# Performance work log

Measured on AMD Instinct MI355X. Metric: run time of the kernel, lower is better.

Reference implementation:

```python
import jax, jax.numpy as jnp
import numpy as np

D_MODEL = 1024
NUM_HEADS = 16
D_K = D_MODEL // NUM_HEADS
B, S = 2, 2048


def setup_inputs() -> dict:
    key = jax.random.key(0)
    ks = jax.random.split(key, 12)
    s = 1.0 / np.sqrt(D_MODEL)
    return {
        "query": jax.random.normal(ks[0], (B, S, D_MODEL), jnp.float32),
        "key": jax.random.normal(ks[1], (B, S, D_MODEL), jnp.float32),
        "value": jax.random.normal(ks[2], (B, S, D_MODEL), jnp.float32),
        "mask": jnp.ones((B, S), jnp.int32),
        "Wq": jax.random.uniform(ks[3], (D_MODEL, D_MODEL), jnp.float32, -s, s),
        "bq": jax.random.uniform(ks[4], (D_MODEL,), jnp.float32, -s, s),
        "Wk": jax.random.uniform(ks[5], (D_MODEL, D_MODEL), jnp.float32, -s, s),
        "bk": jax.random.uniform(ks[6], (D_MODEL,), jnp.float32, -s, s),
        "Wv": jax.random.uniform(ks[7], (D_MODEL, D_MODEL), jnp.float32, -s, s),
        "bv": jax.random.uniform(ks[8], (D_MODEL,), jnp.float32, -s, s),
        "Wo": jax.random.uniform(ks[9], (D_MODEL, D_MODEL), jnp.float32, -s, s),
        "bo": jax.random.uniform(ks[10], (D_MODEL,), jnp.float32, -s, s),
    }


def reference(query, key, value, mask, Wq, bq, Wk, bk, Wv, bv, Wo, bo):
    b, s, _ = query.shape
    scale = jnp.sqrt(jnp.asarray(D_K, jnp.float32)).astype(query.dtype)
    # QKV projections: x @ W.T + b (torch nn.Linear convention)
    Q = (query @ Wq.T + bq).reshape(b, s, NUM_HEADS, D_K).transpose(0, 2, 1, 3)
    K = (key @ Wk.T + bk).reshape(b, -1, NUM_HEADS, D_K).transpose(0, 2, 1, 3)
    V = (value @ Wv.T + bv).reshape(b, -1, NUM_HEADS, D_K).transpose(0, 2, 1, 3)
    # scores in fp32, then cast back to input dtype (matches source)
    scores = jnp.einsum('bhqd,bhkd->bhqk', Q.astype(jnp.float32), K.astype(jnp.float32)) / scale
    scores = scores.astype(Q.dtype)
    # 2D mask [B,S] -> [B,1,1,S], broadcast over heads/queries
    fill = jnp.finfo(scores.dtype).min
    scores = jnp.where(mask[:, None, None, :] == 0, fill, scores)
    attn = jax.nn.softmax(scores, axis=-1)  # dropout p=0 -> identity
    context = jnp.einsum('bhqk,bhkd->bhqd', attn, V)
    context = context.transpose(0, 2, 1, 3).reshape(b, s, D_MODEL)
    return context @ Wo.T + bo
```

## Files before the change

kernel.cpp:

```cpp
#include <hip/hip_runtime.h>


typedef __bf16 bf16_8 __attribute__((ext_vector_type(8)));
typedef float  f32x4  __attribute__((ext_vector_type(4)));
typedef float  f32x16 __attribute__((ext_vector_type(16)));
typedef unsigned int u32x4 __attribute__((ext_vector_type(4)));

#define MFMA16(a, b, c) __builtin_amdgcn_mfma_f32_16x16x32_bf16((a), (b), (c), 0, 0, 0)
#define MFMA32(a, b, c) __builtin_amdgcn_mfma_f32_32x32x16_bf16((a), (b), (c), 0, 0, 0)

__device__ __forceinline__ void async_ld16(const void* g, void* l) {
  __builtin_amdgcn_global_load_lds(
      (__attribute__((address_space(1))) void*)g,
      (__attribute__((address_space(3))) void*)l, 16, 0, 0);
}

__device__ __forceinline__ void gemm_core_128(
    const __bf16* __restrict__ A, const __bf16* __restrict__ BT, int K,
    int tm, int tn, __bf16* At, __bf16* Bt, f32x4 acc[4][4]) {
  const int tid  = threadIdx.x;
  const int lane = tid & 63;
  const int w    = tid >> 6;
  const int quad = lane >> 4;
  const int c16  = lane & 15;
  const int wm = w >> 1, wn = w & 1;

  const int ch0  = w * 2;
  const int row0 = ch0 * 16 + (lane >> 2);
  const int col0 = (lane & 3) * 8;
  const __bf16* Ag = A  + (size_t)(tm + row0) * K + col0;
  const __bf16* Bg = BT + (size_t)(tn + row0) * K + col0;
  __bf16* Al = At + ch0 * 512;
  __bf16* Bl = Bt + ch0 * 512;
  const size_t rowK16 = (size_t)16 * K;

  for (int kt = 0; kt < K; kt += 32) {
    async_ld16(Ag + kt,          Al);
    async_ld16(Ag + rowK16 + kt, Al + 512);
    async_ld16(Bg + kt,          Bl);
    async_ld16(Bg + rowK16 + kt, Bl + 512);
    __syncthreads();

    bf16_8 af[4], bfr[4];
#pragma unroll
    for (int mi = 0; mi < 4; ++mi)
      af[mi] = *(const bf16_8*)(At + (wm * 64 + mi * 16 + c16) * 32 + quad * 8);
#pragma unroll
    for (int ni = 0; ni < 4; ++ni)
      bfr[ni] = *(const bf16_8*)(Bt + (wn * 64 + ni * 16 + c16) * 32 + quad * 8);
#pragma unroll
    for (int mi = 0; mi < 4; ++mi)
#pragma unroll
      for (int ni = 0; ni < 4; ++ni)
        acc[mi][ni] = MFMA16(af[mi], bfr[ni], acc[mi][ni]);
    __syncthreads();
  }
}

__global__ __launch_bounds__(256)
void qkv_fused(const __bf16* __restrict__ xq, const __bf16* __restrict__ xk,
               const __bf16* __restrict__ xv,
               const __bf16* __restrict__ wq, const __bf16* __restrict__ wk,
               const __bf16* __restrict__ wv,
               const float* __restrict__ bq, const float* __restrict__ bk,
               const float* __restrict__ bv,
               __bf16* __restrict__ Qo, __bf16* __restrict__ Ko,
               __bf16* __restrict__ Vo) {
  __shared__ __bf16 At[128 * 32];
  __shared__ __bf16 Bt[128 * 32];
  const int z  = blockIdx.z;
  const int bx = blockIdx.x;
  const __bf16 *A, *BT;
  const float* bias;
  int tm, tn;
  if (z == 2) {
    A = wv; BT = xv; bias = bv;
    tm = (bx >> 5) * 128; tn = (bx & 31) * 128;
  } else if (z == 1) {
    A = xk; BT = wk; bias = bk;
    tm = (bx >> 3) * 128; tn = (bx & 7) * 128;
  } else {
    A = xq; BT = wq; bias = bq;
    tm = (bx >> 3) * 128; tn = (bx & 7) * 128;
  }

  f32x4 acc[4][4];
  const f32x4 zero4 = {0.f, 0.f, 0.f, 0.f};
#pragma unroll
  for (int i = 0; i < 4; ++i)
#pragma unroll
    for (int j = 0; j < 4; ++j) acc[i][j] = zero4;

  gemm_core_128(A, BT, 1024, tm, tn, At, Bt, acc);

  const int lane = threadIdx.x & 63;
  const int w    = threadIdx.x >> 6;
  const int quad = lane >> 4, c16 = lane & 15;
  const int wm = w >> 1, wn = w & 1;

  if (z == 2) {
#pragma unroll
    for (int mi = 0; mi < 4; ++mi) {
#pragma unroll
      for (int ni = 0; ni < 4; ++ni) {
        const int n  = tn + wn * 64 + ni * 16 + c16;
        const int bb = n >> 11, s = n & 2047;
#pragma unroll
        for (int r = 0; r < 4; ++r) {
          const int m  = tm + wm * 64 + mi * 16 + quad * 4 + r;
          const int hh = m >> 6, d = m & 63;
          Vo[(((size_t)(bb * 16 + hh) * 64 + d) << 11) + s] =
              (__bf16)(acc[mi][ni][r] + bias[m]);
        }
      }
    }
  } else {
    __bf16* Out = (z == 1) ? Ko : Qo;
    const float scale = (z == 0) ? 0.125f : 1.0f;
#pragma unroll
    for (int mi = 0; mi < 4; ++mi) {
#pragma unroll
      for (int ni = 0; ni < 4; ++ni) {
        const int n  = tn + wn * 64 + ni * 16 + c16;
        const int hh = n >> 6, d = n & 63;
        const float bn = bias[n];
#pragma unroll
        for (int r = 0; r < 4; ++r) {
          const int m  = tm + wm * 64 + mi * 16 + quad * 4 + r;
          const int bb = m >> 11, s = m & 2047;
          Out[(((size_t)(bb * 16 + hh) * 2048 + s) << 6) + d] =
              (__bf16)((acc[mi][ni][r] + bn) * scale);
        }
      }
    }
  }
}

__global__ __launch_bounds__(256)
void out_proj(const __bf16* __restrict__ ctx, const __bf16* __restrict__ wo,
              const float* __restrict__ bo, float* __restrict__ out) {
  __shared__ __bf16 At[64 * 32];
  __shared__ __bf16 Bt[128 * 32];
  const int bx = blockIdx.x;
  const int tm = (bx >> 3) * 64, tn = (bx & 7) * 128;

  const int tid  = threadIdx.x;
  const int lane = tid & 63, w = tid >> 6;
  const int quad = lane >> 4, c16 = lane & 15;
  const int wm = w >> 1, wn = w & 1;

  const int row0 = lane >> 2, col0 = (lane & 3) * 8;
  const __bf16* Ag = ctx + (size_t)(tm + w * 16 + row0) * 1024 + col0;
  const __bf16* Bg = wo  + (size_t)(tn + w * 32 + row0) * 1024 + col0;
  __bf16* Al = At + w * 512;
  __bf16* Bl = Bt + w * 1024;

  f32x4 acc[2][4];
  const f32x4 zero4 = {0.f, 0.f, 0.f, 0.f};
#pragma unroll
  for (int i = 0; i < 2; ++i)
#pragma unroll
    for (int j = 0; j < 4; ++j) acc[i][j] = zero4;

  for (int kt = 0; kt < 1024; kt += 32) {
    async_ld16(Ag + kt, Al);
    async_ld16(Bg + kt, Bl);
    async_ld16(Bg + 16 * 1024 + kt, Bl + 512);
    __syncthreads();

    bf16_8 af[2], bfr[4];
#pragma unroll
    for (int mi = 0; mi < 2; ++mi)
      af[mi] = *(const bf16_8*)(At + (wm * 32 + mi * 16 + c16) * 32 + quad * 8);
#pragma unroll
    for (int ni = 0; ni < 4; ++ni)
      bfr[ni] = *(const bf16_8*)(Bt + (wn * 64 + ni * 16 + c16) * 32 + quad * 8);
#pragma unroll
    for (int mi = 0; mi < 2; ++mi)
#pragma unroll
      for (int ni = 0; ni < 4; ++ni)
        acc[mi][ni] = MFMA16(af[mi], bfr[ni], acc[mi][ni]);
    __syncthreads();
  }

#pragma unroll
  for (int mi = 0; mi < 2; ++mi) {
#pragma unroll
    for (int ni = 0; ni < 4; ++ni) {
      const int n = tn + wn * 64 + ni * 16 + c16;
      const float bn = bo[n];
#pragma unroll
      for (int r = 0; r < 4; ++r) {
        const int m = tm + wm * 32 + mi * 16 + quad * 4 + r;
        out[(size_t)m * 1024 + n] = acc[mi][ni][r] + bn;
      }
    }
  }
}

__global__ __launch_bounds__(512, 4)
void flash_attn(const __bf16* __restrict__ Qg, const __bf16* __restrict__ Kg,
                const __bf16* __restrict__ VTg, const int* __restrict__ maskg,
                __bf16* __restrict__ ctx) {
  __shared__ __align__(16) char smem_[76288];

  const int t    = threadIdx.x;
  const int lane = t & 63;
  const int w    = t >> 6;
  const int g    = w & 3;
  const int hh   = w >> 2;
  const int n32  = lane & 31;
  const int h    = lane >> 5;

  const int linear = blockIdx.x + (blockIdx.y << 4) + (blockIdx.z << 8);
  const int sw     = (linear & 7) * 64 + (linear >> 3);
  const int qt     = sw & 15;
  const int head   = (sw >> 4) & 15;
  const int b      = sw >> 8;

  const size_t bh = (size_t)(b * 16 + head);
  const int qbase = qt * 128 + g * 32;

  bf16_8 bq[4];
  {
    const __bf16* qptr = Qg + (bh * 2048 + qbase + n32) * 64 + h * 8;
#pragma unroll
    for (int s = 0; s < 4; ++s) bq[s] = *(const bf16_8*)(qptr + s * 16);
  }

  const f32x16 z16 = {0.f,0.f,0.f,0.f,0.f,0.f,0.f,0.f,
                      0.f,0.f,0.f,0.f,0.f,0.f,0.f,0.f};
  f32x16 o0 = z16, o1 = z16;
  float lsum = 0.f;

  const int tl   = t & 255;
  const int srow = tl >> 2, scc = (tl & 3) * 16;
  const __bf16* Kgp = Kg  + (bh * 2048 + hh * 1024) * 64;
  const __bf16* Vgp = VTg + bh * 64 * 2048 + hh * 1024;
  const int*    mgp = maskg + b * 2048 + hh * 1024;
  const float LOG2E = 1.44269504088896f;

  __bf16* const Kb0 = (__bf16*)smem_;
  __bf16* const Vb0 = (__bf16*)(smem_ + 36864);
  float*  const Mb0 = (float*)(smem_ + 73728);

  bf16_8 rk0, rk1, rv0, rv1;
  int rmv;

#define FA_ISSUE(KT) do {                                         \
    const size_t kb_ = (size_t)((KT) + srow) * 64 + scc;          \
    rk0 = *(const bf16_8*)&Kgp[kb_];                              \
    rk1 = *(const bf16_8*)&Kgp[kb_ + 8];                          \
    const size_t vb_ = (size_t)srow * 2048 + (KT) + scc;          \
    rv0 = *(const bf16_8*)&Vgp[vb_];                              \
    rv1 = *(const bf16_8*)&Vgp[vb_ + 8];                          \
    if (tl < 64) rmv = mgp[(KT) + tl];                            \
  } while (0)

  FA_ISSUE(0);

  for (int it = 0; it < 16; ++it) {
    const int cur = it & 1;
    __bf16* const Klc = Kb0 + (cur * 2 + hh) * 4608;
    __bf16* const Vlc = Vb0 + (cur * 2 + hh) * 4608;
    float*  const Mlc = Mb0 + (cur * 2 + hh) * 64;

    {
      __bf16* kw = Klc + srow * 72 + scc;
      *(bf16_8*)kw       = rk0;
      *(bf16_8*)(kw + 8) = rk1;
      __bf16* vw = Vlc + srow * 72 + scc;
      *(bf16_8*)vw       = rv0;
      *(bf16_8*)(vw + 8) = rv1;
      if (tl < 64) Mlc[tl] = rmv ? -17.3123404907f : -1e30f;
    }
    if (it + 1 < 16) FA_ISSUE((it + 1) * 64);

    __syncthreads();

#pragma unroll
    for (int kt2 = 0; kt2 < 2; ++kt2) {
      f32x4 ma4[4];
#pragma unroll
      for (int j = 0; j < 4; ++j)
        ma4[j] = *(const f32x4*)&Mlc[kt2 * 32 + 8 * j + 4 * h];

      f32x16 p = z16;
      __builtin_amdgcn_s_setprio(1);
#pragma unroll
      for (int s = 0; s < 4; ++s) {
        const bf16_8 ka =
            *(const bf16_8*)&Klc[(kt2 * 32 + n32) * 72 + s * 16 + h * 8];
        p = MFMA32(ka, bq[s], p);
      }
      __builtin_amdgcn_s_setprio(0);

      unsigned c[8];
#pragma unroll
      for (int i = 0; i < 8; ++i) {
        const int r0 = 2 * i, r1 = 2 * i + 1;
        const float e0 =
            __builtin_amdgcn_exp2f(fmaf(p[r0], LOG2E, ma4[r0 >> 2][r0 & 3]));
        const float e1 =
            __builtin_amdgcn_exp2f(fmaf(p[r1], LOG2E, ma4[r1 >> 2][r1 & 3]));
        lsum += e0 + e1;
        union { __bf16 hx[2]; unsigned u; } uu;
        uu.hx[0] = (__bf16)e0;
        uu.hx[1] = (__bf16)e1;
        c[i] = uu.u;
      }
      asm volatile("v_permlane32_swap_b32 %0, %1" : "+v"(c[0]), "+v"(c[2]));
      asm volatile("v_permlane32_swap_b32 %0, %1" : "+v"(c[1]), "+v"(c[3]));
      asm volatile("v_permlane32_swap_b32 %0, %1" : "+v"(c[4]), "+v"(c[6]));
      asm volatile("v_permlane32_swap_b32 %0, %1" : "+v"(c[5]), "+v"(c[7]));

#pragma unroll
      for (int sub = 0; sub < 2; ++sub) {
        const u32x4 av = {c[4 * sub + 0], c[4 * sub + 1],
                          c[4 * sub + 2], c[4 * sub + 3]};
        const bf16_8 aP = __builtin_bit_cast(bf16_8, av);
        const int s = kt2 * 2 + sub;
        const bf16_8 vb0 =
            *(const bf16_8*)&Vlc[n32 * 72 + s * 16 + h * 8];
        const bf16_8 vb1 =
            *(const bf16_8*)&Vlc[(32 + n32) * 72 + s * 16 + h * 8];
        __builtin_amdgcn_s_setprio(1);
        o0 = MFMA32(aP, vb0, o0);
        o1 = MFMA32(aP, vb1, o1);
        __builtin_amdgcn_s_setprio(0);
      }
    }
  }
#undef FA_ISSUE

  lsum += __shfl_xor(lsum, 32);

  __syncthreads();

  float (*Om)[32][64] = (float(*)[32][64])smem_;
  float (*Lm)[32]     = (float(*)[32])(smem_ + 75776);

  if (hh) {
#pragma unroll
    for (int r = 0; r < 16; ++r) {
      const int qrow = (r & 3) + 8 * (r >> 2) + 4 * h;
      Om[g][qrow][n32]      = o0[r];
      Om[g][qrow][32 + n32] = o1[r];
    }
    if (h == 0) Lm[g][n32] = lsum;
  }
  __syncthreads();
  if (!hh) {
    const float linv = 1.0f / (lsum + Lm[g][n32]);
#pragma unroll
    for (int r = 0; r < 16; ++r) {
      const int qrow = (r & 3) + 8 * (r >> 2) + 4 * h;
      const float li = __shfl(linv, qrow);
      __bf16* cp = ctx + ((size_t)b * 2048 + qbase + qrow) * 1024 + head * 64;
      cp[n32]      = (__bf16)((o0[r] + Om[g][qrow][n32]) * li);
      cp[32 + n32] = (__bf16)((o1[r] + Om[g][qrow][32 + n32]) * li);
    }
  }
}

__global__ __launch_bounds__(256)
void cvt_all(const float* __restrict__ q, const float* __restrict__ k,
             const float* __restrict__ v, const float* __restrict__ Wq,
             const float* __restrict__ Wk, const float* __restrict__ Wv,
             const float* __restrict__ Wo,
             __bf16* __restrict__ xq, __bf16* __restrict__ xk,
             __bf16* __restrict__ xv, __bf16* __restrict__ wqb,
             __bf16* __restrict__ wkb, __bf16* __restrict__ wvb,
             __bf16* __restrict__ wob) {
  const int y = blockIdx.y;
  const float* s;
  __bf16* d;
  int n8;
  switch (y) {
    case 0: s = q;  d = xq;  n8 = 524288; break;
    case 1: s = k;  d = xk;  n8 = 524288; break;
    case 2: s = v;  d = xv;  n8 = 524288; break;
    case 3: s = Wq; d = wqb; n8 = 131072; break;
    case 4: s = Wk; d = wkb; n8 = 131072; break;
    case 5: s = Wv; d = wvb; n8 = 131072; break;
    default: s = Wo; d = wob; n8 = 131072; break;
  }
  const int i = blockIdx.x * blockDim.x + threadIdx.x;
  if (i < n8) {
    const float4* sp = (const float4*)s;
    const float4 v0 = sp[i * 2], v1 = sp[i * 2 + 1];
    bf16_8 o;
    o[0] = (__bf16)v0.x; o[1] = (__bf16)v0.y;
    o[2] = (__bf16)v0.z; o[3] = (__bf16)v0.w;
    o[4] = (__bf16)v1.x; o[5] = (__bf16)v1.y;
    o[6] = (__bf16)v1.z; o[7] = (__bf16)v1.w;
    *(bf16_8*)(d + (size_t)i * 8) = o;
  }
}

extern "C" void kernel_launch(void* const* d_in, const int* in_sizes, int n_in,
                              void* d_out, int out_size, void* d_ws, size_t ws_size,
                              hipStream_t stream) {
  (void)in_sizes; (void)n_in; (void)out_size; (void)ws_size;
  const float* q    = (const float*)d_in[0];
  const float* k    = (const float*)d_in[1];
  const float* v    = (const float*)d_in[2];
  const int*   mask = (const int*)d_in[3];
  const float* Wq = (const float*)d_in[4];
  const float* bq = (const float*)d_in[5];
  const float* Wk = (const float*)d_in[6];
  const float* bk = (const float*)d_in[7];
  const float* Wv = (const float*)d_in[8];
  const float* bv = (const float*)d_in[9];
  const float* Wo = (const float*)d_in[10];
  const float* bo = (const float*)d_in[11];

  char* ws = (char*)d_ws;
  const size_t MB = 1ull << 20;
  __bf16* xq  = (__bf16*)(ws + 0 * MB);
  __bf16* xk  = (__bf16*)(ws + 8 * MB);
  __bf16* xv  = (__bf16*)(ws + 16 * MB);
  __bf16* wqb = (__bf16*)(ws + 24 * MB);
  __bf16* wkb = (__bf16*)(ws + 26 * MB);
  __bf16* wvb = (__bf16*)(ws + 28 * MB);
  __bf16* wob = (__bf16*)(ws + 30 * MB);
  __bf16* Qb  = (__bf16*)(ws + 32 * MB);
  __bf16* Kb  = (__bf16*)(ws + 40 * MB);
  __bf16* VTb = (__bf16*)(ws + 48 * MB);
  __bf16* ctx = (__bf16*)(ws + 56 * MB);

  cvt_all<<<dim3(2048, 7), 256, 0, stream>>>(q, k, v, Wq, Wk, Wv, Wo,
                                             xq, xk, xv, wqb, wkb, wvb, wob);

  qkv_fused<<<dim3(256, 1, 3), 256, 0, stream>>>(xq, xk, xv, wqb, wkb, wvb,
                                                 bq, bk, bv, Qb, Kb, VTb);

  flash_attn<<<dim3(16, 16, 2), 512, 0, stream>>>(Qb, Kb, VTb, mask, ctx);

  out_proj<<<dim3(512), 256, 0, stream>>>(ctx, wob, bo, (float*)d_out);
}
```

Before: 221.0 us.

## Fold log2e into Q scale, compute row sums via MFMA, remap tile order

The Q projection scale now includes log2(e), so the attention kernel seeds the MFMA accumulator with the mask bias and applies exp2 directly, without a per-element FMA. Softmax row sums are now computed by an extra MFMA against a ones vector rather than scalar adds plus a shuffle. The main loop is manually unrolled by two with pointer-increment loads, and the setprio hints are removed. Block index swizzles are added to the QKV and output projection GEMMs to change tile traversal order for cache locality. The row sums are now taken from the bf16-rounded probabilities, and the extra MFMA per step adds matrix-unit work.

```diff
diff --git a/kernel.cpp b/kernel.cpp
--- a/kernel.cpp
+++ b/kernel.cpp
@@ -68,14 +68,15 @@
                __bf16* __restrict__ Vo) {
   __shared__ __bf16 At[128 * 32];
   __shared__ __bf16 Bt[128 * 32];
-  const int z  = blockIdx.z;
-  const int bx = blockIdx.x;
+  const int z   = blockIdx.z;
+  const int bx0 = blockIdx.x;
+  const int bx  = ((bx0 & 7) << 5) | (bx0 >> 3);
   const __bf16 *A, *BT;
   const float* bias;
   int tm, tn;
   if (z == 2) {
     A = wv; BT = xv; bias = bv;
-    tm = (bx >> 5) * 128; tn = (bx & 31) * 128;
+    tm = (bx & 7) * 128; tn = (bx >> 3) * 128;
   } else if (z == 1) {
     A = xk; BT = wk; bias = bk;
     tm = (bx >> 3) * 128; tn = (bx & 7) * 128;
@@ -116,7 +117,7 @@
     }
   } else {
     __bf16* Out = (z == 1) ? Ko : Qo;
-    const float scale = (z == 0) ? 0.125f : 1.0f;
+    const float scale = (z == 0) ? 0.1803368801f : 1.0f;
 #pragma unroll
     for (int mi = 0; mi < 4; ++mi) {
 #pragma unroll
@@ -141,7 +142,8 @@
               const float* __restrict__ bo, float* __restrict__ out) {
   __shared__ __bf16 At[64 * 32];
   __shared__ __bf16 Bt[128 * 32];
-  const int bx = blockIdx.x;
+  const int bx0 = blockIdx.x;
+  const int bx  = ((bx0 & 7) << 6) | (bx0 >> 3);
   const int tm = (bx >> 3) * 64, tn = (bx & 7) * 128;
 
   const int tid  = threadIdx.x;
@@ -228,42 +230,46 @@
     for (int s = 0; s < 4; ++s) bq[s] = *(const bf16_8*)(qptr + s * 16);
   }
 
+  bf16_8 onesb;
+#pragma unroll
+  for (int i = 0; i < 8; ++i) onesb[i] = (__bf16)1.0f;
+
   const f32x16 z16 = {0.f,0.f,0.f,0.f,0.f,0.f,0.f,0.f,
                       0.f,0.f,0.f,0.f,0.f,0.f,0.f,0.f};
   f32x16 o0 = z16, o1 = z16;
-  float lsum = 0.f;
+  f32x16 ls = z16;
 
   const int tl   = t & 255;
   const int srow = tl >> 2, scc = (tl & 3) * 16;
   const __bf16* Kgp = Kg  + (bh * 2048 + hh * 1024) * 64;
   const __bf16* Vgp = VTg + bh * 64 * 2048 + hh * 1024;
   const int*    mgp = maskg + b * 2048 + hh * 1024;
-  const float LOG2E = 1.44269504088896f;
 
   __bf16* const Kb0 = (__bf16*)smem_;
   __bf16* const Vb0 = (__bf16*)(smem_ + 36864);
   float*  const Mb0 = (float*)(smem_ + 73728);
 
   bf16_8 rk0, rk1, rv0, rv1;
-  int rmv;
-
-#define FA_ISSUE(KT) do {                                         \
-    const size_t kb_ = (size_t)((KT) + srow) * 64 + scc;          \
-    rk0 = *(const bf16_8*)&Kgp[kb_];                              \
-    rk1 = *(const bf16_8*)&Kgp[kb_ + 8];                          \
-    const size_t vb_ = (size_t)srow * 2048 + (KT) + scc;          \
-    rv0 = *(const bf16_8*)&Vgp[vb_];                              \
-    rv1 = *(const bf16_8*)&Vgp[vb_ + 8];                          \
-    if (tl < 64) rmv = mgp[(KT) + tl];                            \
-  } while (0)
-
-  FA_ISSUE(0);
-
-  for (int it = 0; it < 16; ++it) {
-    const int cur = it & 1;
-    __bf16* const Klc = Kb0 + (cur * 2 + hh) * 4608;
-    __bf16* const Vlc = Vb0 + (cur * 2 + hh) * 4608;
-    float*  const Mlc = Mb0 + (cur * 2 + hh) * 64;
+  int rmv = 0;
+  const __bf16* kS = Kgp + (size_t)srow * 64 + scc;
+  const __bf16* vS = Vgp + (size_t)srow * 2048 + scc;
+  const int*    mS = mgp + tl;
+
+  auto fa_issue = [&]() {
+    rk0 = *(const bf16_8*)kS;
+    rk1 = *(const bf16_8*)(kS + 8);
+    rv0 = *(const bf16_8*)vS;
+    rv1 = *(const bf16_8*)(vS + 8);
+    if (tl < 64) rmv = *mS;
+    kS += 64 * 64;
+    vS += 64;
+    mS += 64;
+  };
+
+  auto fa_body = [&](int CUR, int IT) {
+    __bf16* const Klc = Kb0 + (CUR * 2 + hh) * 4608;
+    __bf16* const Vlc = Vb0 + (CUR * 2 + hh) * 4608;
+    float*  const Mlc = Mb0 + (CUR * 2 + hh) * 64;
 
     {
       __bf16* kw = Klc + srow * 72 + scc;
@@ -274,36 +280,33 @@
       *(bf16_8*)(vw + 8) = rv1;
       if (tl < 64) Mlc[tl] = rmv ? -17.3123404907f : -1e30f;
     }
-    if (it + 1 < 16) FA_ISSUE((it + 1) * 64);
+    if (IT < 15) fa_issue();
 
     __syncthreads();
 
 #pragma unroll
     for (int kt2 = 0; kt2 < 2; ++kt2) {
-      f32x4 ma4[4];
-#pragma unroll
-      for (int j = 0; j < 4; ++j)
-        ma4[j] = *(const f32x4*)&Mlc[kt2 * 32 + 8 * j + 4 * h];
-
-      f32x16 p = z16;
-      __builtin_amdgcn_s_setprio(1);
+      f32x16 p;
+#pragma unroll
+      for (int j = 0; j < 4; ++j) {
+        const f32x4 m4 = *(const f32x4*)&Mlc[kt2 * 32 + 8 * j + 4 * h];
+        p[4 * j + 0] = m4[0];
+        p[4 * j + 1] = m4[1];
+        p[4 * j + 2] = m4[2];
+        p[4 * j + 3] = m4[3];
+      }
 #pragma unroll
       for (int s = 0; s < 4; ++s) {
         const bf16_8 ka =
             *(const bf16_8*)&Klc[(kt2 * 32 + n32) * 72 + s * 16 + h * 8];
         p = MFMA32(ka, bq[s], p);
       }
-      __builtin_amdgcn_s_setprio(0);
 
       unsigned c[8];
 #pragma unroll
       for (int i = 0; i < 8; ++i) {
-        const int r0 = 2 * i, r1 = 2 * i + 1;
-        const float e0 =
-            __builtin_amdgcn_exp2f(fmaf(p[r0], LOG2E, ma4[r0 >> 2][r0 & 3]));
-        const float e1 =
-            __builtin_amdgcn_exp2f(fmaf(p[r1], LOG2E, ma4[r1 >> 2][r1 & 3]));
-        lsum += e0 + e1;
+        const float e0 = __builtin_amdgcn_exp2f(p[2 * i]);
+        const float e1 = __builtin_amdgcn_exp2f(p[2 * i + 1]);
         union { __bf16 hx[2]; unsigned u; } uu;
         uu.hx[0] = (__bf16)e0;
         uu.hx[1] = (__bf16)e1;
@@ -324,16 +327,19 @@
             *(const bf16_8*)&Vlc[n32 * 72 + s * 16 + h * 8];
         const bf16_8 vb1 =
             *(const bf16_8*)&Vlc[(32 + n32) * 72 + s * 16 + h * 8];
-        __builtin_amdgcn_s_setprio(1);
         o0 = MFMA32(aP, vb0, o0);
         o1 = MFMA32(aP, vb1, o1);
-        __builtin_amdgcn_s_setprio(0);
-      }
-    }
-  }
-#undef FA_ISSUE
-
-  lsum += __shfl_xor(lsum, 32);
+        ls = MFMA32(aP, onesb, ls);
+      }
+    }
+  };
+
+  fa_issue();
+#pragma unroll 1
+  for (int it2 = 0; it2 < 8; ++it2) {
+    fa_body(0, it2 * 2);
+    fa_body(1, it2 * 2 + 1);
+  }
 
   __syncthreads();
 
@@ -347,18 +353,21 @@
       Om[g][qrow][n32]      = o0[r];
       Om[g][qrow][32 + n32] = o1[r];
     }
-    if (h == 0) Lm[g][n32] = lsum;
+    if (n32 == 0) {
+#pragma unroll
+      for (int r = 0; r < 16; ++r)
+        Lm[g][(r & 3) + 8 * (r >> 2) + 4 * h] = ls[r];
+    }
   }
   __syncthreads();
   if (!hh) {
-    const float linv = 1.0f / (lsum + Lm[g][n32]);
 #pragma unroll
     for (int r = 0; r < 16; ++r) {
       const int qrow = (r & 3) + 8 * (r >> 2) + 4 * h;
-      const float li = __shfl(linv, qrow);
+      const float linv = 1.0f / (ls[r] + Lm[g][qrow]);
       __bf16* cp = ctx + ((size_t)b * 2048 + qbase + qrow) * 1024 + head * 64;
-      cp[n32]      = (__bf16)((o0[r] + Om[g][qrow][n32]) * li);
-      cp[32 + n32] = (__bf16)((o1[r] + Om[g][qrow][32 + n32]) * li);
+      cp[n32]      = (__bf16)((o0[r] + Om[g][qrow][n32]) * linv);
+      cp[32 + n32] = (__bf16)((o1[r] + Om[g][qrow][32 + n32]) * linv);
     }
   }
 }
```

Result: no change. 223.9 us (+1.3%).
